# Performance work log

Measured on AMD Instinct MI355X. Metric: run time of the kernel, lower is better.

The kernel has to match this reference:

```python
import jax, jax.numpy as jnp
import numpy as np

N = 100000   # nodes
E = 1600000  # edges
D_IN, H1, H2, H3 = 128, 128, 128, 64


def _sage_layer(x, src, dst, Wl, Wr, b):
    # PyG SAGEConv (aggr='mean'): out = lin_l(mean_{j in N(i)} x_j) + lin_r(x_i)
    msg_sum = jax.ops.segment_sum(x[src], dst, num_segments=N)          # [N, F]
    deg = jax.ops.segment_sum(jnp.ones((src.shape[0],), x.dtype), dst, num_segments=N)
    mean = msg_sum / jnp.clip(deg, 1.0)[:, None]
    return mean @ Wl + x @ Wr + b


def setup_inputs() -> dict:
    key = jax.random.key(0)
    ks = jax.random.split(key, 11)
    x = jax.random.normal(ks[0], (N, D_IN), dtype=jnp.float32)
    edge_index = jax.random.randint(ks[1], (2, E), 0, N, dtype=jnp.int32)

    def w(k, fin, fout):
        return jax.random.normal(k, (fin, fout), dtype=jnp.float32) * (1.0 / np.sqrt(fin))

    return {
        "x": x,
        "edge_index": edge_index,
        "W1_l": w(ks[2], D_IN, H1), "W1_r": w(ks[3], D_IN, H1), "b1": jnp.zeros((H1,), jnp.float32),
        "W2_l": w(ks[4], H1, H2),  "W2_r": w(ks[5], H1, H2),  "b2": jnp.zeros((H2,), jnp.float32),
        "W3_l": w(ks[6], H2, H3),  "W3_r": w(ks[7], H2, H3),  "b3": jnp.zeros((H3,), jnp.float32),
    }


def reference(x, edge_index, W1_l, W1_r, b1, W2_l, W2_r, b2, W3_l, W3_r, b3):
    src, dst = edge_index[0], edge_index[1]
    h = jax.nn.relu(_sage_layer(x, src, dst, W1_l, W1_r, b1))
    h = jax.nn.relu(_sage_layer(h, src, dst, W2_l, W2_r, b2))
    return _sage_layer(h, src, dst, W3_l, W3_r, b3)
```

## Files before the change

### kernel.cpp

```cpp
#include <hip/hip_runtime.h>

#define NN 100000
#define NE 1600000
#define NPB 256
#define NB 391
#define CAP 4864
#define NBLK_A 512
#define CHUNK_A (NE / NBLK_A)
#define CVT_N (NN * 16)

typedef __attribute__((ext_vector_type(8))) short bf16x8;
typedef __attribute__((ext_vector_type(4))) float f32x4;


__device__ __forceinline__ unsigned short f2bf(float f) {
    unsigned int u = __float_as_uint(f);
    unsigned int r = u + 0x7fffu + ((u >> 16) & 1u);
    return (unsigned short)(r >> 16);
}
__device__ __forceinline__ float bflo(unsigned int u) { return __uint_as_float(u << 16); }
__device__ __forceinline__ float bfhi(unsigned int u) { return __uint_as_float(u & 0xffff0000u); }
__device__ __forceinline__ unsigned int packbf(float lo, float hi) {
    return ((unsigned int)f2bf(hi) << 16) | (unsigned int)f2bf(lo);
}
__device__ __forceinline__ bf16x8 as_bf8(uint4 u) {
    union { uint4 u; bf16x8 h; } c;
    c.u = u;
    return c.h;
}


__global__ __launch_bounds__(256) void bucket_scatter_kernel(
    const int* __restrict__ src, const int* __restrict__ dst,
    int* __restrict__ gcur, unsigned* __restrict__ buckets) {
    __shared__ int hist[NB];
    __shared__ int base[NB];
    int t = threadIdx.x;
    for (int b = t; b < NB; b += 256) hist[b] = 0;
    __syncthreads();
    int e0 = blockIdx.x * CHUNK_A;
    for (int e = e0 + t; e < e0 + CHUNK_A; e += 256)
        atomicAdd(&hist[dst[e] >> 8], 1);
    __syncthreads();
    for (int b = t; b < NB; b += 256) {
        base[b] = atomicAdd(&gcur[b], hist[b]);
        hist[b] = 0;
    }
    __syncthreads();
    for (int e = e0 + t; e < e0 + CHUNK_A; e += 256) {
        int d = dst[e];
        int bkt = d >> 8;
        int slot = base[bkt] + atomicAdd(&hist[bkt], 1);
        if (slot < CAP)
            buckets[(size_t)bkt * CAP + slot] =
                ((unsigned)(d & 255) << 24) | (unsigned)src[e];
    }
}


__global__ __launch_bounds__(512) void bucket_scan_kernel(
    const int* __restrict__ gcur, int* __restrict__ bstart, int* __restrict__ row_ptr) {
    __shared__ int s[512];
    int t = threadIdx.x;
    int v = (t < NB) ? gcur[t] : 0;
    s[t] = v;
    __syncthreads();
    for (int off = 1; off < 512; off <<= 1) {
        int a = (t >= off) ? s[t - off] : 0;
        __syncthreads();
        s[t] += a;
        __syncthreads();
    }
    if (t < NB) bstart[t] = s[t] - v;
    if (t == NB - 1) {
        bstart[NB] = s[t];
        row_ptr[NN] = s[t];
    }
}


__global__ __launch_bounds__(256) void csr_finalize_kernel(
    const unsigned* __restrict__ buckets, const int* __restrict__ gcur,
    const int* __restrict__ bstart, int* __restrict__ row_ptr, int* __restrict__ adj) {
    __shared__ int hist[NPB];
    __shared__ int scn[NPB];
    int b = blockIdx.x;
    int t = threadIdx.x;
    int n = gcur[b];
    if (n > CAP) n = CAP;
    int base = bstart[b];
    const unsigned* bk = buckets + (size_t)b * CAP;

    hist[t] = 0;
    __syncthreads();
    for (int i = t; i < n; i += 256) atomicAdd(&hist[bk[i] >> 24], 1);
    __syncthreads();

    int v = hist[t];
    scn[t] = v;
    __syncthreads();
    for (int off = 1; off < 256; off <<= 1) {
        int add = (t >= off) ? scn[t - off] : 0;
        __syncthreads();
        scn[t] += add;
        __syncthreads();
    }
    int excl = scn[t] - v;
    int node = b * NPB + t;
    if (node < NN) row_ptr[node] = base + excl;

    hist[t] = excl;
    __syncthreads();
    for (int i = t; i < n; i += 256) {
        unsigned pr = bk[i];
        int pos = atomicAdd(&hist[pr >> 24], 1);
        adj[base + pos] = (int)(pr & 0xFFFFFFu);
    }
}


__device__ __forceinline__ void wfrag_one(const float* __restrict__ W, int H, int idx,
                                          uint4* __restrict__ out) {
    int lane = idx & 63;
    int tile = idx >> 6;
    int ntiles = H >> 4;
    int nt = tile % ntiles;
    int kt = tile / ntiles;
    int kbase = kt * 32 + (lane >> 4) * 8;
    int col = nt * 16 + (lane & 15);
    uint4 r;
    r.x = packbf(W[(size_t)(kbase + 0) * H + col], W[(size_t)(kbase + 1) * H + col]);
    r.y = packbf(W[(size_t)(kbase + 2) * H + col], W[(size_t)(kbase + 3) * H + col]);
    r.z = packbf(W[(size_t)(kbase + 4) * H + col], W[(size_t)(kbase + 5) * H + col]);
    r.w = packbf(W[(size_t)(kbase + 6) * H + col], W[(size_t)(kbase + 7) * H + col]);
    out[idx] = r;
}

__global__ __launch_bounds__(256) void prep_kernel(
    const float* __restrict__ x, unsigned int* __restrict__ x_bf,
    const float* __restrict__ W1l, const float* __restrict__ W1r,
    const float* __restrict__ W2l, const float* __restrict__ W2r,
    const float* __restrict__ W3l, const float* __restrict__ W3r,
    uint4* __restrict__ wf1, uint4* __restrict__ wf2,
    uint4* __restrict__ wf3l, uint4* __restrict__ wf3r) {
    int idx = blockIdx.x * blockDim.x + threadIdx.x;
    if (idx < CVT_N) {
        const float4* p = (const float4*)x + (size_t)idx * 2;
        float4 a = p[0], b = p[1];
        uint4 r;
        r.x = packbf(a.x, a.y);
        r.y = packbf(a.z, a.w);
        r.z = packbf(b.x, b.y);
        r.w = packbf(b.z, b.w);
        ((uint4*)x_bf)[idx] = r;
    } else {
        int k = idx - CVT_N;
        if (k < 2048)       wfrag_one(W1l, 128, k, wf1);
        else if (k < 4096)  wfrag_one(W1r, 128, k - 2048, wf1 + 2048);
        else if (k < 6144)  wfrag_one(W2l, 128, k - 4096, wf2);
        else if (k < 8192)  wfrag_one(W2r, 128, k - 6144, wf2 + 2048);
        else if (k < 9216)  wfrag_one(W3l, 64, k - 8192, wf3l);
        else if (k < 10240) wfrag_one(W3r, 64, k - 9216, wf3r);
    }
}


__global__ __launch_bounds__(256) void pull128_kernel(
    const uint4* __restrict__ xb4, const int* __restrict__ row_ptr,
    const int* __restrict__ adj, uint4* __restrict__ aggb4) {
    int node = blockIdx.x * 4 + (threadIdx.x >> 6);
    int l = threadIdx.x & 63;
    int g = l >> 4;
    int i = l & 15;
    int beg = row_ptr[node], end = row_ptr[node + 1];
    float acc[8];
#pragma unroll
    for (int j = 0; j < 8; ++j) acc[j] = 0.f;

    int p = beg;
    for (; p + 16 <= end; p += 16) {
#pragma unroll
        for (int j = 0; j < 4; ++j) {
            int s = adj[p + j * 4 + g];
            uint4 u = xb4[(size_t)s * 16 + i];
            acc[0] += bflo(u.x);
            acc[1] += bfhi(u.x);
            acc[2] += bflo(u.y);
            acc[3] += bfhi(u.y);
            acc[4] += bflo(u.z);
            acc[5] += bfhi(u.z);
            acc[6] += bflo(u.w);
            acc[7] += bfhi(u.w);
        }
    }
    if (p < end) {
#pragma unroll
        for (int j = 0; j < 4; ++j) {
            int e = p + j * 4 + g;
            bool vv = e < end;
            int s = vv ? adj[e] : 0;
            uint4 u = xb4[(size_t)s * 16 + i];
            float m = vv ? 1.f : 0.f;
            acc[0] = fmaf(m, bflo(u.x), acc[0]);
            acc[1] = fmaf(m, bfhi(u.x), acc[1]);
            acc[2] = fmaf(m, bflo(u.y), acc[2]);
            acc[3] = fmaf(m, bfhi(u.y), acc[3]);
            acc[4] = fmaf(m, bflo(u.z), acc[4]);
            acc[5] = fmaf(m, bfhi(u.z), acc[5]);
            acc[6] = fmaf(m, bflo(u.w), acc[6]);
            acc[7] = fmaf(m, bfhi(u.w), acc[7]);
        }
    }

#pragma unroll
    for (int j = 0; j < 8; ++j) {
        acc[j] += __shfl_xor(acc[j], 16);
        acc[j] += __shfl_xor(acc[j], 32);
    }
    if (g == 0) {
        float inv = 1.0f / (float)(end > beg ? (end - beg) : 1);
        uint4 r;
        r.x = packbf(acc[0] * inv, acc[1] * inv);
        r.y = packbf(acc[2] * inv, acc[3] * inv);
        r.z = packbf(acc[4] * inv, acc[5] * inv);
        r.w = packbf(acc[6] * inv, acc[7] * inv);
        aggb4[(size_t)node * 16 + i] = r;
    }
}


__global__ __launch_bounds__(256) void pull64_kernel(
    const uint2* __restrict__ zb2, const int* __restrict__ row_ptr,
    const int* __restrict__ adj, float* __restrict__ aggout) {
    int node = blockIdx.x * 4 + (threadIdx.x >> 6);
    int l = threadIdx.x & 63;
    int g = l >> 4;
    int i = l & 15;
    int beg = row_ptr[node], end = row_ptr[node + 1];
    float acc[4];
#pragma unroll
    for (int j = 0; j < 4; ++j) acc[j] = 0.f;

    int p = beg;
    for (; p + 16 <= end; p += 16) {
#pragma unroll
        for (int j = 0; j < 4; ++j) {
            int s = adj[p + j * 4 + g];
            uint2 u = zb2[(size_t)s * 16 + i];
            acc[0] += bflo(u.x);
            acc[1] += bfhi(u.x);
            acc[2] += bflo(u.y);
            acc[3] += bfhi(u.y);
        }
    }
    if (p < end) {
#pragma unroll
        for (int j = 0; j < 4; ++j) {
            int e = p + j * 4 + g;
            bool vv = e < end;
            int s = vv ? adj[e] : 0;
            uint2 u = zb2[(size_t)s * 16 + i];
            float m = vv ? 1.f : 0.f;
            acc[0] = fmaf(m, bflo(u.x), acc[0]);
            acc[1] = fmaf(m, bfhi(u.x), acc[1]);
            acc[2] = fmaf(m, bflo(u.y), acc[2]);
            acc[3] = fmaf(m, bfhi(u.y), acc[3]);
        }
    }

#pragma unroll
    for (int j = 0; j < 4; ++j) {
        acc[j] += __shfl_xor(acc[j], 16);
        acc[j] += __shfl_xor(acc[j], 32);
    }
    if (g == 0) {
        float inv = 1.0f / (float)(end > beg ? (end - beg) : 1);
        float4 r;
        r.x = acc[0] * inv;
        r.y = acc[1] * inv;
        r.z = acc[2] * inv;
        r.w = acc[3] * inv;
        *(float4*)(aggout + (size_t)node * 64 + i * 4) = r;
    }
}


template <bool FUSE_Z>
__global__ __launch_bounds__(256) void sage_mfma_kernel(
    const uint4* __restrict__ aggA, const uint4* __restrict__ xinA,
    const uint4* __restrict__ wfrag, const float* __restrict__ bias,
    unsigned short* __restrict__ outb,
    const uint4* __restrict__ wfz, unsigned short* __restrict__ zout) {
    extern __shared__ unsigned short hts[];

    const int w = threadIdx.x >> 6;
    const int l = threadIdx.x & 63;
    const int r0 = blockIdx.x * 64 + w * 16;
    int arow = r0 + (l & 15);
    if (arow > NN - 1) arow = NN - 1;
    const int koff = l >> 4;

    f32x4 acc[8];
#pragma unroll
    for (int nt = 0; nt < 8; ++nt) {
        f32x4 z = {0.f, 0.f, 0.f, 0.f};
        acc[nt] = z;
    }

#pragma unroll
    for (int kt = 0; kt < 8; ++kt) {
        const uint4* Ab = (kt < 4) ? aggA : xinA;
        const int ktl = kt & 3;
        bf16x8 av = as_bf8(Ab[(size_t)arow * 16 + ktl * 4 + koff]);
#pragma unroll
        for (int nt = 0; nt < 8; ++nt) {
            bf16x8 bv = as_bf8(wfrag[(kt * 8 + nt) * 64 + l]);
            acc[nt] = __builtin_amdgcn_mfma_f32_16x16x32_bf16(av, bv, acc[nt], 0, 0, 0);
        }
    }

    const int crow0 = r0 + ((l >> 4) << 2);
    const int ccol = l & 15;
#pragma unroll
    for (int nt = 0; nt < 8; ++nt) {
        float bb = bias[nt * 16 + ccol];
#pragma unroll
        for (int q = 0; q < 4; ++q) {
            int r = crow0 + q;
            unsigned short hb = f2bf(fmaxf(acc[nt][q] + bb, 0.f));
            if (r < NN) outb[(size_t)r * 128 + nt * 16 + ccol] = hb;
            if (FUSE_Z) {
                hts[((size_t)w * 16 + ((l >> 4) << 2) + q) * 136 + nt * 16 + ccol] = hb;
            }
        }
    }

    if (FUSE_Z) {
        __syncthreads();
        f32x4 accz[4];
#pragma unroll
        for (int nt = 0; nt < 4; ++nt) {
            f32x4 z = {0.f, 0.f, 0.f, 0.f};
            accz[nt] = z;
        }
#pragma unroll
        for (int kt = 0; kt < 4; ++kt) {
            const uint4 hv =
                *(const uint4*)&hts[((size_t)w * 16 + (l & 15)) * 136 + kt * 32 + (l >> 4) * 8];
            bf16x8 av = as_bf8(hv);
#pragma unroll
            for (int nt = 0; nt < 4; ++nt) {
                bf16x8 bv = as_bf8(wfz[(kt * 4 + nt) * 64 + l]);
                accz[nt] = __builtin_amdgcn_mfma_f32_16x16x32_bf16(av, bv, accz[nt], 0, 0, 0);
            }
        }
#pragma unroll
        for (int nt = 0; nt < 4; ++nt) {
#pragma unroll
            for (int q = 0; q < 4; ++q) {
                int r = crow0 + q;
                if (r < NN) zout[(size_t)r * 64 + nt * 16 + ccol] = f2bf(accz[nt][q]);
            }
        }
    }
}


__global__ __launch_bounds__(256) void mm64_final_kernel(
    const uint4* __restrict__ A, const uint4* __restrict__ wfrag,
    const float* __restrict__ addin, const float* __restrict__ bias,
    float* __restrict__ out) {
    const int w = threadIdx.x >> 6;
    const int l = threadIdx.x & 63;
    const int r0 = blockIdx.x * 64 + w * 16;
    int arow = r0 + (l & 15);
    if (arow > NN - 1) arow = NN - 1;
    const int koff = l >> 4;

    f32x4 acc[4];
#pragma unroll
    for (int nt = 0; nt < 4; ++nt) {
        f32x4 z = {0.f, 0.f, 0.f, 0.f};
        acc[nt] = z;
    }

#pragma unroll
    for (int kt = 0; kt < 4; ++kt) {
        bf16x8 av = as_bf8(A[(size_t)arow * 16 + kt * 4 + koff]);
#pragma unroll
        for (int nt = 0; nt < 4; ++nt) {
            bf16x8 bv = as_bf8(wfrag[(kt * 4 + nt) * 64 + l]);
            acc[nt] = __builtin_amdgcn_mfma_f32_16x16x32_bf16(av, bv, acc[nt], 0, 0, 0);
        }
    }

    const int crow0 = r0 + ((l >> 4) << 2);
    const int ccol = l & 15;
#pragma unroll
    for (int nt = 0; nt < 4; ++nt) {
        int col = nt * 16 + ccol;
#pragma unroll
        for (int q = 0; q < 4; ++q) {
            int r = crow0 + q;
            if (r < NN) {
                out[(size_t)r * 64 + col] =
                    acc[nt][q] + addin[(size_t)r * 64 + col] + bias[col];
            }
        }
    }
}


extern "C" void kernel_launch(void* const* d_in, const int* in_sizes, int n_in,
                              void* d_out, int out_size, void* d_ws, size_t ws_size,
                              hipStream_t stream) {
    (void)in_sizes; (void)n_in; (void)out_size; (void)ws_size;

    const float* x   = (const float*)d_in[0];
    const int* eidx  = (const int*)d_in[1];
    const int* src   = eidx;
    const int* dst   = eidx + NE;
    const float* W1l = (const float*)d_in[2];
    const float* W1r = (const float*)d_in[3];
    const float* b1  = (const float*)d_in[4];
    const float* W2l = (const float*)d_in[5];
    const float* W2r = (const float*)d_in[6];
    const float* b2  = (const float*)d_in[7];
    const float* W3l = (const float*)d_in[8];
    const float* W3r = (const float*)d_in[9];
    const float* b3  = (const float*)d_in[10];
    float* out = (float*)d_out;

    size_t off = 0;
    auto carve = [&](size_t bytes) -> void* {
        void* p = (char*)d_ws + off;
        off += (bytes + 255) & ~(size_t)255;
        return p;
    };
    int* gcur    = (int*)carve((size_t)NB * 4);
    int* bstart  = (int*)carve((size_t)(NB + 1) * 4);
    int* row_ptr = (int*)carve((size_t)(NN + 1) * 4);
    int* adj     = (int*)carve((size_t)NE * 4);
    unsigned* buckets = (unsigned*)carve((size_t)NB * CAP * 4);
    unsigned int* x_bf  = (unsigned int*)carve((size_t)NN * 64 * 4);
    unsigned int* agg   = (unsigned int*)carve((size_t)NN * 64 * 4);
    unsigned int* h1_bf = (unsigned int*)carve((size_t)NN * 64 * 4);
    unsigned int* h2_bf = (unsigned int*)carve((size_t)NN * 64 * 4);
    unsigned int* z_bf  = (unsigned int*)carve((size_t)NN * 32 * 4);
    float* agg3         = (float*)carve((size_t)NN * 64 * 4);
    uint4* wf1  = (uint4*)carve((size_t)8 * 8 * 64 * 16);
    uint4* wf2  = (uint4*)carve((size_t)8 * 8 * 64 * 16);
    uint4* wf3l = (uint4*)carve((size_t)4 * 4 * 64 * 16);
    uint4* wf3r = (uint4*)carve((size_t)4 * 4 * 64 * 16);

    const int pgrid = (NN + 3) / 4;
    const int mgrid = (NN + 63) / 64;
    const int cgrid = (CVT_N + 10240) / 256;

    hipMemsetAsync(gcur, 0, (size_t)NB * 4, stream);
    bucket_scatter_kernel<<<NBLK_A, 256, 0, stream>>>(src, dst, gcur, buckets);
    bucket_scan_kernel<<<1, 512, 0, stream>>>(gcur, bstart, row_ptr);
    csr_finalize_kernel<<<NB, 256, 0, stream>>>(buckets, gcur, bstart, row_ptr, adj);

    prep_kernel<<<cgrid, 256, 0, stream>>>(x, x_bf, W1l, W1r, W2l, W2r, W3l, W3r,
                                           wf1, wf2, wf3l, wf3r);

    pull128_kernel<<<pgrid, 256, 0, stream>>>((const uint4*)x_bf, row_ptr, adj, (uint4*)agg);
    sage_mfma_kernel<false><<<mgrid, 256, 0, stream>>>(
        (const uint4*)agg, (const uint4*)x_bf, wf1, b1, (unsigned short*)h1_bf,
        nullptr, nullptr);
    pull128_kernel<<<pgrid, 256, 0, stream>>>((const uint4*)h1_bf, row_ptr, adj, (uint4*)agg);
    sage_mfma_kernel<true><<<mgrid, 256, 4 * 16 * 136 * 2, stream>>>(
        (const uint4*)agg, (const uint4*)h1_bf, wf2, b2, (unsigned short*)h2_bf,
        wf3l, (unsigned short*)z_bf);
    pull64_kernel<<<pgrid, 256, 0, stream>>>((const uint2*)z_bf, row_ptr, adj, agg3);
    mm64_final_kernel<<<mgrid, 256, 0, stream>>>((const uint4*)h2_bf, wf3r, agg3, b3, out);
}
```

Before: 300.6 us.

## Fuse bucket scatter with prep, fold scan into finalize, one node per quarter-wave pull

Merges the edge bucket-scatter and the x/weight bf16 conversion into a single launch, and removes the separate scan kernel by having each finalize block reduce the prefix of bucket counts itself. The pull kernels now give each 16-lane group its own node, walking its edges four at a time instead of splitting edges across groups and reducing with shuffles. This cuts launches and cross-lane reductions, at the cost of redundant prefix sums per block and more per-lane load imbalance across nodes.

```diff
diff --git a/kernel.cpp b/kernel.cpp
--- a/kernel.cpp
+++ b/kernel.cpp
@@ -8,6 +8,7 @@
 #define NBLK_A 512
 #define CHUNK_A (NE / NBLK_A)
 #define CVT_N (NN * 16)
+#define PREP_BLKS ((CVT_N + 10240) / 256)
 
 typedef __attribute__((ext_vector_type(8))) short bf16x8;
 typedef __attribute__((ext_vector_type(4))) float f32x4;
@@ -27,95 +28,6 @@
     union { uint4 u; bf16x8 h; } c;
     c.u = u;
     return c.h;
-}
-
-
-__global__ __launch_bounds__(256) void bucket_scatter_kernel(
-    const int* __restrict__ src, const int* __restrict__ dst,
-    int* __restrict__ gcur, unsigned* __restrict__ buckets) {
-    __shared__ int hist[NB];
-    __shared__ int base[NB];
-    int t = threadIdx.x;
-    for (int b = t; b < NB; b += 256) hist[b] = 0;
-    __syncthreads();
-    int e0 = blockIdx.x * CHUNK_A;
-    for (int e = e0 + t; e < e0 + CHUNK_A; e += 256)
-        atomicAdd(&hist[dst[e] >> 8], 1);
-    __syncthreads();
-    for (int b = t; b < NB; b += 256) {
-        base[b] = atomicAdd(&gcur[b], hist[b]);
-        hist[b] = 0;
-    }
-    __syncthreads();
-    for (int e = e0 + t; e < e0 + CHUNK_A; e += 256) {
-        int d = dst[e];
-        int bkt = d >> 8;
-        int slot = base[bkt] + atomicAdd(&hist[bkt], 1);
-        if (slot < CAP)
-            buckets[(size_t)bkt * CAP + slot] =
-                ((unsigned)(d & 255) << 24) | (unsigned)src[e];
-    }
-}
-
-
-__global__ __launch_bounds__(512) void bucket_scan_kernel(
-    const int* __restrict__ gcur, int* __restrict__ bstart, int* __restrict__ row_ptr) {
-    __shared__ int s[512];
-    int t = threadIdx.x;
-    int v = (t < NB) ? gcur[t] : 0;
-    s[t] = v;
-    __syncthreads();
-    for (int off = 1; off < 512; off <<= 1) {
-        int a = (t >= off) ? s[t - off] : 0;
-        __syncthreads();
-        s[t] += a;
-        __syncthreads();
-    }
-    if (t < NB) bstart[t] = s[t] - v;
-    if (t == NB - 1) {
-        bstart[NB] = s[t];
-        row_ptr[NN] = s[t];
-    }
-}
-
-
-__global__ __launch_bounds__(256) void csr_finalize_kernel(
-    const unsigned* __restrict__ buckets, const int* __restrict__ gcur,
-    const int* __restrict__ bstart, int* __restrict__ row_ptr, int* __restrict__ adj) {
-    __shared__ int hist[NPB];
-    __shared__ int scn[NPB];
-    int b = blockIdx.x;
-    int t = threadIdx.x;
-    int n = gcur[b];
-    if (n > CAP) n = CAP;
-    int base = bstart[b];
-    const unsigned* bk = buckets + (size_t)b * CAP;
-
-    hist[t] = 0;
-    __syncthreads();
-    for (int i = t; i < n; i += 256) atomicAdd(&hist[bk[i] >> 24], 1);
-    __syncthreads();
-
-    int v = hist[t];
-    scn[t] = v;
-    __syncthreads();
-    for (int off = 1; off < 256; off <<= 1) {
-        int add = (t >= off) ? scn[t - off] : 0;
-        __syncthreads();
-        scn[t] += add;
-        __syncthreads();
-    }
-    int excl = scn[t] - v;
-    int node = b * NPB + t;
-    if (node < NN) row_ptr[node] = base + excl;
-
-    hist[t] = excl;
-    __syncthreads();
-    for (int i = t; i < n; i += 256) {
-        unsigned pr = bk[i];
-        int pos = atomicAdd(&hist[pr >> 24], 1);
-        adj[base + pos] = (int)(pr & 0xFFFFFFu);
-    }
 }
 
 
@@ -136,31 +48,111 @@
     out[idx] = r;
 }
 
-__global__ __launch_bounds__(256) void prep_kernel(
+
+__global__ __launch_bounds__(256) void scatter_prep_kernel(
+    const int* __restrict__ src, const int* __restrict__ dst,
+    int* __restrict__ gcur, unsigned* __restrict__ buckets,
     const float* __restrict__ x, unsigned int* __restrict__ x_bf,
     const float* __restrict__ W1l, const float* __restrict__ W1r,
     const float* __restrict__ W2l, const float* __restrict__ W2r,
     const float* __restrict__ W3l, const float* __restrict__ W3r,
     uint4* __restrict__ wf1, uint4* __restrict__ wf2,
     uint4* __restrict__ wf3l, uint4* __restrict__ wf3r) {
-    int idx = blockIdx.x * blockDim.x + threadIdx.x;
-    if (idx < CVT_N) {
-        const float4* p = (const float4*)x + (size_t)idx * 2;
-        float4 a = p[0], b = p[1];
-        uint4 r;
-        r.x = packbf(a.x, a.y);
-        r.y = packbf(a.z, a.w);
-        r.z = packbf(b.x, b.y);
-        r.w = packbf(b.z, b.w);
-        ((uint4*)x_bf)[idx] = r;
+    __shared__ int hist[NB];
+    __shared__ int base[NB];
+    int t = threadIdx.x;
+
+    if (blockIdx.x < NBLK_A) {
+        for (int b = t; b < NB; b += 256) hist[b] = 0;
+        __syncthreads();
+        int e0 = blockIdx.x * CHUNK_A;
+        for (int e = e0 + t; e < e0 + CHUNK_A; e += 256)
+            atomicAdd(&hist[dst[e] >> 8], 1);
+        __syncthreads();
+        for (int b = t; b < NB; b += 256) {
+            base[b] = atomicAdd(&gcur[b], hist[b]);
+            hist[b] = 0;
+        }
+        __syncthreads();
+        for (int e = e0 + t; e < e0 + CHUNK_A; e += 256) {
+            int d = dst[e];
+            int bkt = d >> 8;
+            int slot = base[bkt] + atomicAdd(&hist[bkt], 1);
+            if (slot < CAP)
+                buckets[(size_t)bkt * CAP + slot] =
+                    ((unsigned)(d & 255) << 24) | (unsigned)src[e];
+        }
     } else {
-        int k = idx - CVT_N;
-        if (k < 2048)       wfrag_one(W1l, 128, k, wf1);
-        else if (k < 4096)  wfrag_one(W1r, 128, k - 2048, wf1 + 2048);
-        else if (k < 6144)  wfrag_one(W2l, 128, k - 4096, wf2);
-        else if (k < 8192)  wfrag_one(W2r, 128, k - 6144, wf2 + 2048);
-        else if (k < 9216)  wfrag_one(W3l, 64, k - 8192, wf3l);
-        else if (k < 10240) wfrag_one(W3r, 64, k - 9216, wf3r);
+        int idx = (blockIdx.x - NBLK_A) * 256 + t;
+        if (idx < CVT_N) {
+            const float4* p = (const float4*)x + (size_t)idx * 2;
+            float4 a = p[0], b = p[1];
+            uint4 r;
+            r.x = packbf(a.x, a.y);
+            r.y = packbf(a.z, a.w);
+            r.z = packbf(b.x, b.y);
+            r.w = packbf(b.z, b.w);
+            ((uint4*)x_bf)[idx] = r;
+        } else {
+            int k = idx - CVT_N;
+            if (k < 2048)       wfrag_one(W1l, 128, k, wf1);
+            else if (k < 4096)  wfrag_one(W1r, 128, k - 2048, wf1 + 2048);
+            else if (k < 6144)  wfrag_one(W2l, 128, k - 4096, wf2);
+            else if (k < 8192)  wfrag_one(W2r, 128, k - 6144, wf2 + 2048);
+            else if (k < 9216)  wfrag_one(W3l, 64, k - 8192, wf3l);
+            else if (k < 10240) wfrag_one(W3r, 64, k - 9216, wf3r);
+        }
+    }
+}
+
+
+__global__ __launch_bounds__(256) void csr_finalize_kernel(
+    const unsigned* __restrict__ buckets, const int* __restrict__ gcur,
+    int* __restrict__ row_ptr, int* __restrict__ adj) {
+    __shared__ int hist[NPB];
+    __shared__ int scn[NPB];
+    int b = blockIdx.x;
+    int t = threadIdx.x;
+
+    int part = 0;
+    for (int j = t; j < b; j += 256) part += gcur[j];
+    scn[t] = part;
+    __syncthreads();
+    for (int off = 128; off > 0; off >>= 1) {
+        if (t < off) scn[t] += scn[t + off];
+        __syncthreads();
+    }
+    int base = scn[0];
+
+    int nraw = gcur[b];
+    int n = (nraw > CAP) ? CAP : nraw;
+    if (b == NB - 1 && t == 0) row_ptr[NN] = base + nraw;
+    const unsigned* bk = buckets + (size_t)b * CAP;
+
+    hist[t] = 0;
+    __syncthreads();
+    for (int i = t; i < n; i += 256) atomicAdd(&hist[bk[i] >> 24], 1);
+    __syncthreads();
+
+    int v = hist[t];
+    scn[t] = v;
+    __syncthreads();
+    for (int off = 1; off < 256; off <<= 1) {
+        int add = (t >= off) ? scn[t - off] : 0;
+        __syncthreads();
+        scn[t] += add;
+        __syncthreads();
+    }
+    int excl = scn[t] - v;
+    int node = b * NPB + t;
+    if (node < NN) row_ptr[node] = base + excl;
+
+    hist[t] = excl;
+    __syncthreads();
+    for (int i = t; i < n; i += 256) {
+        unsigned pr = bk[i];
+        int pos = atomicAdd(&hist[pr >> 24], 1);
+        adj[base + pos] = (int)(pr & 0xFFFFFFu);
     }
 }
 
@@ -168,120 +160,97 @@
 __global__ __launch_bounds__(256) void pull128_kernel(
     const uint4* __restrict__ xb4, const int* __restrict__ row_ptr,
     const int* __restrict__ adj, uint4* __restrict__ aggb4) {
-    int node = blockIdx.x * 4 + (threadIdx.x >> 6);
-    int l = threadIdx.x & 63;
-    int g = l >> 4;
-    int i = l & 15;
-    int beg = row_ptr[node], end = row_ptr[node + 1];
+    const int l = threadIdx.x & 63;
+    const int g = l >> 4;
+    const int i = l & 15;
+    const int node = blockIdx.x * 16 + (threadIdx.x >> 6) * 4 + g;
+    const int beg = row_ptr[node], end = row_ptr[node + 1];
+
     float acc[8];
 #pragma unroll
     for (int j = 0; j < 8; ++j) acc[j] = 0.f;
 
     int p = beg;
-    for (; p + 16 <= end; p += 16) {
-#pragma unroll
-        for (int j = 0; j < 4; ++j) {
-            int s = adj[p + j * 4 + g];
-            uint4 u = xb4[(size_t)s * 16 + i];
-            acc[0] += bflo(u.x);
-            acc[1] += bfhi(u.x);
-            acc[2] += bflo(u.y);
-            acc[3] += bfhi(u.y);
-            acc[4] += bflo(u.z);
-            acc[5] += bfhi(u.z);
-            acc[6] += bflo(u.w);
-            acc[7] += bfhi(u.w);
-        }
-    }
-    if (p < end) {
-#pragma unroll
-        for (int j = 0; j < 4; ++j) {
-            int e = p + j * 4 + g;
-            bool vv = e < end;
-            int s = vv ? adj[e] : 0;
-            uint4 u = xb4[(size_t)s * 16 + i];
-            float m = vv ? 1.f : 0.f;
-            acc[0] = fmaf(m, bflo(u.x), acc[0]);
-            acc[1] = fmaf(m, bfhi(u.x), acc[1]);
-            acc[2] = fmaf(m, bflo(u.y), acc[2]);
-            acc[3] = fmaf(m, bfhi(u.y), acc[3]);
-            acc[4] = fmaf(m, bflo(u.z), acc[4]);
-            acc[5] = fmaf(m, bfhi(u.z), acc[5]);
-            acc[6] = fmaf(m, bflo(u.w), acc[6]);
-            acc[7] = fmaf(m, bfhi(u.w), acc[7]);
-        }
-    }
-
-#pragma unroll
-    for (int j = 0; j < 8; ++j) {
-        acc[j] += __shfl_xor(acc[j], 16);
-        acc[j] += __shfl_xor(acc[j], 32);
-    }
-    if (g == 0) {
-        float inv = 1.0f / (float)(end > beg ? (end - beg) : 1);
-        uint4 r;
-        r.x = packbf(acc[0] * inv, acc[1] * inv);
-        r.y = packbf(acc[2] * inv, acc[3] * inv);
-        r.z = packbf(acc[4] * inv, acc[5] * inv);
-        r.w = packbf(acc[6] * inv, acc[7] * inv);
-        aggb4[(size_t)node * 16 + i] = r;
-    }
+    for (; p + 4 <= end; p += 4) {
+        int s0 = adj[p + 0], s1 = adj[p + 1], s2 = adj[p + 2], s3 = adj[p + 3];
+        uint4 u0 = xb4[(size_t)s0 * 16 + i];
+        uint4 u1 = xb4[(size_t)s1 * 16 + i];
+        uint4 u2 = xb4[(size_t)s2 * 16 + i];
+        uint4 u3 = xb4[(size_t)s3 * 16 + i];
+        acc[0] += (bflo(u0.x) + bflo(u1.x)) + (bflo(u2.x) + bflo(u3.x));
+        acc[1] += (bfhi(u0.x) + bfhi(u1.x)) + (bfhi(u2.x) + bfhi(u3.x));
+        acc[2] += (bflo(u0.y) + bflo(u1.y)) + (bflo(u2.y) + bflo(u3.y));
+        acc[3] += (bfhi(u0.y) + bfhi(u1.y)) + (bfhi(u2.y) + bfhi(u3.y));
+        acc[4] += (bflo(u0.z) + bflo(u1.z)) + (bflo(u2.z) + bflo(u3.z));
+        acc[5] += (bfhi(u0.z) + bfhi(u1.z)) + (bfhi(u2.z) + bfhi(u3.z));
+        acc[6] += (bflo(u0.w) + bflo(u1.w)) + (bflo(u2.w) + bflo(u3.w));
+        acc[7] += (bfhi(u0.w) + bfhi(u1.w)) + (bfhi(u2.w) + bfhi(u3.w));
+    }
+    for (; p < end; ++p) {
+        uint4 u = xb4[(size_t)adj[p] * 16 + i];
+        acc[0] += bflo(u.x);
+        acc[1] += bfhi(u.x);
+        acc[2] += bflo(u.y);
+        acc[3] += bfhi(u.y);
+        acc[4] += bflo(u.z);
+        acc[5] += bfhi(u.z);
+        acc[6] += bflo(u.w);
+        acc[7] += bfhi(u.w);
+    }
+
+    float inv = 1.0f / (float)(end > beg ? (end - beg) : 1);
+    uint4 r;
+    r.x = packbf(acc[0] * inv, acc[1] * inv);
+    r.y = packbf(acc[2] * inv, acc[3] * inv);
+    r.z = packbf(acc[4] * inv, acc[5] * inv);
+    r.w = packbf(acc[6] * inv, acc[7] * inv);
+    aggb4[(size_t)node * 16 + i] = r;
 }
 
 
 __global__ __launch_bounds__(256) void pull64_kernel(
     const uint2* __restrict__ zb2, const int* __restrict__ row_ptr,
     const int* __restrict__ adj, float* __restrict__ aggout) {
-    int node = blockIdx.x * 4 + (threadIdx.x >> 6);
-    int l = threadIdx.x & 63;
-    int g = l >> 4;
-    int i = l & 15;
-    int beg = row_ptr[node], end = row_ptr[node + 1];
+    const int l = threadIdx.x & 63;
+    const int g = l >> 4;
+    const int i = l & 15;
+    const int node = blockIdx.x * 16 + (threadIdx.x >> 6) * 4 + g;
+    const int beg = row_ptr[node], end = row_ptr[node + 1];
+
     float acc[4];
 #pragma unroll
     for (int j = 0; j < 4; ++j) acc[j] = 0.f;
 
     int p = beg;
-    for (; p + 16 <= end; p += 16) {
-#pragma unroll
-        for (int j = 0; j < 4; ++j) {
-            int s = adj[p + j * 4 + g];
-            uint2 u = zb2[(size_t)s * 16 + i];
-            acc[0] += bflo(u.x);
-            acc[1] += bfhi(u.x);
-            acc[2] += bflo(u.y);
-            acc[3] += bfhi(u.y);
-        }
-    }
-    if (p < end) {
-#pragma unroll
-        for (int j = 0; j < 4; ++j) {
-            int e = p + j * 4 + g;
-            bool vv = e < end;
-            int s = vv ? adj[e] : 0;
-            uint2 u = zb2[(size_t)s * 16 + i];
-            float m = vv ? 1.f : 0.f;
-            acc[0] = fmaf(m, bflo(u.x), acc[0]);
-            acc[1] = fmaf(m, bfhi(u.x), acc[1]);
-            acc[2] = fmaf(m, bflo(u.y), acc[2]);
-            acc[3] = fmaf(m, bfhi(u.y), acc[3]);
-        }
-    }
-
-#pragma unroll
-    for (int j = 0; j < 4; ++j) {
-        acc[j] += __shfl_xor(acc[j], 16);
-        acc[j] += __shfl_xor(acc[j], 32);
-    }
-    if (g == 0) {
-        float inv = 1.0f / (float)(end > beg ? (end - beg) : 1);
-        float4 r;
-        r.x = acc[0] * inv;
-        r.y = acc[1] * inv;
-        r.z = acc[2] * inv;
-        r.w = acc[3] * inv;
-        *(float4*)(aggout + (size_t)node * 64 + i * 4) = r;
-    }
+    for (; p + 4 <= end; p += 4) {
+        int s0 = adj[p + 0], s1 = adj[p + 1], s2 = adj[p + 2], s3 = adj[p + 3];
+        uint2 u0 = zb2[(size_t)s0 * 16 + i];
+        uint2 u1 = zb2[(size_t)s1 * 16 + i];
+        uint2 u2 = zb2[(size_t)s2 * 16 + i];
+        uint2 u3 = zb2[(size_t)s3 * 16 + i];
+        acc[0] += (bflo(u0.x) + bflo(u1.x)) + (bflo(u2.x) + bflo(u3.x));
+        acc[1] += (bfhi(u0.x) + bfhi(u1.x)) + (bfhi(u2.x) + bfhi(u3.x));
+        acc[2] += (bflo(u0.y) + bflo(u1.y)) + (bflo(u2.y) + bflo(u3.y));
+        acc[3] += (bfhi(u0.y) + bfhi(u1.y)) + (bfhi(u2.y) + bfhi(u3.y));
+    }
+    for (; p < end; ++p) {
+        uint2 u = zb2[(size_t)adj[p] * 16 + i];
+        acc[0] += bflo(u.x);
+        acc[1] += bfhi(u.x);
+        acc[2] += bflo(u.y);
+        acc[3] += bfhi(u.y);
+    }
+
+    float inv = 1.0f / (float)(end > beg ? (end - beg) : 1);
+    float2 r;
+    r.x = acc[0] * inv;
+    r.y = acc[1] * inv;
+    float2 r2;
+    r2.x = acc[2] * inv;
+    r2.y = acc[3] * inv;
+    float4 w;
+    w.x = r.x; w.y = r.y; w.z = r2.x; w.w = r2.y;
+    *(float4*)(aggout + (size_t)node * 64 + i * 4) = w;
 }
 
 
@@ -438,7 +407,6 @@
         return p;
     };
     int* gcur    = (int*)carve((size_t)NB * 4);
-    int* bstart  = (int*)carve((size_t)(NB + 1) * 4);
     int* row_ptr = (int*)carve((size_t)(NN + 1) * 4);
     int* adj     = (int*)carve((size_t)NE * 4);
     unsigned* buckets = (unsigned*)carve((size_t)NB * CAP * 4);
@@ -453,17 +421,14 @@
     uint4* wf3l = (uint4*)carve((size_t)4 * 4 * 64 * 16);
     uint4* wf3r = (uint4*)carve((size_t)4 * 4 * 64 * 16);
 
-    const int pgrid = (NN + 3) / 4;
+    const int pgrid = NN / 16;
     const int mgrid = (NN + 63) / 64;
-    const int cgrid = (CVT_N + 10240) / 256;
 
     hipMemsetAsync(gcur, 0, (size_t)NB * 4, stream);
-    bucket_scatter_kernel<<<NBLK_A, 256, 0, stream>>>(src, dst, gcur, buckets);
-    bucket_scan_kernel<<<1, 512, 0, stream>>>(gcur, bstart, row_ptr);
-    csr_finalize_kernel<<<NB, 256, 0, stream>>>(buckets, gcur, bstart, row_ptr, adj);
-
-    prep_kernel<<<cgrid, 256, 0, stream>>>(x, x_bf, W1l, W1r, W2l, W2r, W3l, W3r,
-                                           wf1, wf2, wf3l, wf3r);
+    scatter_prep_kernel<<<NBLK_A + PREP_BLKS, 256, 0, stream>>>(
+        src, dst, gcur, buckets, x, x_bf, W1l, W1r, W2l, W2r, W3l, W3r,
+        wf1, wf2, wf3l, wf3r);
+    csr_finalize_kernel<<<NB, 256, 0, stream>>>(buckets, gcur, row_ptr, adj);
 
     pull128_kernel<<<pgrid, 256, 0, stream>>>((const uint4*)x_bf, row_ptr, adj, (uint4*)agg);
     sage_mfma_kernel<false><<<mgrid, 256, 0, stream>>>(
```

Result: no change. 301.2 us (+0.2%).
